# Optimization experiments

Hardware: AMD Instinct MI355X
Metric: run time of the kernel (lower is better)

## Reference

```python
import jax, jax.numpy as jnp
import numpy as np

DIM = 1024
NUM_HEADS = 16
NUM_KV_HEADS = 4
HEAD_DIM = DIM // NUM_HEADS
KV_DIM = NUM_KV_HEADS * HEAD_DIM
PARTIAL_ROPE_DIM = 32
ROPE_BASE = 10000.0
LORA_RANK = 4
NUM_LORA_STEPS = 2
LORA_SCALE = 1.0
B, S = 2, 2048


def _rms_norm(x):
    eps = jnp.asarray(jnp.finfo(x.dtype).eps, x.dtype)
    return x * jax.lax.rsqrt(jnp.mean(x * x, axis=-1, keepdims=True) + eps)


def _rope_cos_sin(seq_len, dtype):
    half = PARTIAL_ROPE_DIM // 2
    inv_freq = 1.0 / (ROPE_BASE ** (jnp.arange(0, PARTIAL_ROPE_DIM, 2, dtype=jnp.float32) / PARTIAL_ROPE_DIM))
    t = jnp.arange(seq_len, dtype=jnp.float32)
    freqs = jnp.outer(t, inv_freq)  # [S, half]
    return jnp.cos(freqs).astype(dtype), jnp.sin(freqs).astype(dtype)


def _apply_rope_partial(x, cos, sin):
    # x: [B, H, S, D]; rotate first PARTIAL_ROPE_DIM dims, pass the rest.
    half = PARTIAL_ROPE_DIM // 2
    x1 = x[..., :half]
    x2 = x[..., half:PARTIAL_ROPE_DIM]
    xp = x[..., PARTIAL_ROPE_DIM:]
    c = cos[None, None, :, :]
    s = sin[None, None, :, :]
    return jnp.concatenate([x1 * c + x2 * s, -x1 * s + x2 * c, xp], axis=-1)


def setup_inputs() -> dict:
    key = jax.random.key(0)
    ks = jax.random.split(key, 12)
    std = 0.02
    return {
        "x": jax.random.normal(ks[0], (B, S, DIM), jnp.float32),
        "Wq": jax.random.normal(ks[1], (DIM, DIM), jnp.float32) * std,
        "Wk": jax.random.normal(ks[2], (KV_DIM, DIM), jnp.float32) * std,
        "Wv": jax.random.normal(ks[3], (KV_DIM, DIM), jnp.float32) * std,
        "Wproj": jax.random.normal(ks[4], (DIM, DIM), jnp.float32) * std,
        "q_gain": jnp.full((NUM_HEADS,), 1.0, jnp.float32),
        "lora_A_q": jax.random.normal(ks[5], (NUM_LORA_STEPS, LORA_RANK, DIM), jnp.float32) * std,
        "lora_B_q": jax.random.normal(ks[6], (NUM_LORA_STEPS, DIM, LORA_RANK), jnp.float32) * std,
        "lora_A_v": jax.random.normal(ks[7], (NUM_LORA_STEPS, LORA_RANK, DIM), jnp.float32) * std,
        "lora_B_v": jax.random.normal(ks[8], (NUM_LORA_STEPS, KV_DIM, LORA_RANK), jnp.float32) * std,
        "step_idx": 0,
    }


def reference(x, Wq, Wk, Wv, Wproj, q_gain, lora_A_q, lora_B_q, lora_A_v, lora_B_v, step_idx):
    bsz, seqlen, dim = x.shape
    q = x @ Wq.T
    v = x @ Wv.T
    if 0 <= step_idx < NUM_LORA_STEPS:
        q = q + LORA_SCALE * ((x @ lora_A_q[step_idx].T) @ lora_B_q[step_idx].T)
        v = v + LORA_SCALE * ((x @ lora_A_v[step_idx].T) @ lora_B_v[step_idx].T)
    k = x @ Wk.T

    q = q.reshape(bsz, seqlen, NUM_HEADS, HEAD_DIM).transpose(0, 2, 1, 3)      # [B,H,S,D]
    k = k.reshape(bsz, seqlen, NUM_KV_HEADS, HEAD_DIM).transpose(0, 2, 1, 3)   # [B,Hkv,S,D]
    v = v.reshape(bsz, seqlen, NUM_KV_HEADS, HEAD_DIM).transpose(0, 2, 1, 3)

    q = _rms_norm(q)
    k = _rms_norm(k)

    cos, sin = _rope_cos_sin(seqlen, q.dtype)
    q = _apply_rope_partial(q, cos, sin)
    k = _apply_rope_partial(k, cos, sin)

    q = q * q_gain.astype(q.dtype)[None, :, None, None]

    # GQA causal SDPA
    groups = NUM_HEADS // NUM_KV_HEADS
    qg = q.reshape(bsz, NUM_KV_HEADS, groups, seqlen, HEAD_DIM)
    scale = 1.0 / np.sqrt(HEAD_DIM)
    scores = jnp.einsum('bkgsd,bktd->bkgst', qg, k) * scale  # [B,Hkv,G,S,S]
    causal = jnp.tril(jnp.ones((seqlen, seqlen), bool))
    scores = jnp.where(causal[None, None, None], scores, jnp.asarray(-jnp.inf, scores.dtype))
    attn = jax.nn.softmax(scores, axis=-1)
    y = jnp.einsum('bkgst,bktd->bkgsd', attn, v)
    y = y.reshape(bsz, NUM_HEADS, seqlen, HEAD_DIM).transpose(0, 2, 1, 3).reshape(bsz, seqlen, dim)
    return y @ Wproj.T
```

## Files before the change

kernel.cpp:

```cpp
#include <hip/hip_runtime.h>
#include <hip/hip_bf16.h>
#include <stdint.h>

#define DIM 1024
#define NH 16
#define NKV 4
#define HD 64
#define SEQ 2048
#define BATCH 2
#define RANK 4
#define NSTEPS 2

#define XN      4194304
#define WQ_END  5242880
#define WK_END  5505024
#define WV_END  5767168
#define CVT_BLOCKS 6656
#define LORA_BLOCKS 1024

typedef unsigned short u16;
typedef unsigned int u32;
typedef __attribute__((ext_vector_type(8))) __bf16 bf16x8;
typedef __attribute__((ext_vector_type(4))) float f32x4;

__device__ __forceinline__ float bf2f(u16 v) {
    u32 u = ((u32)v) << 16;
    return __builtin_bit_cast(float, u);
}
__device__ __forceinline__ u16 f2bf(float f) {
    u32 u = __builtin_bit_cast(u32, f);
    u32 r = (u + 0x7fffu + ((u >> 16) & 1u)) >> 16;
    return (u16)r;
}
__device__ __forceinline__ u32 pk2(float a, float b) {
    return (u32)f2bf(a) | ((u32)f2bf(b) << 16);
}
__device__ __forceinline__ u32 pk2t(float a, float b) {
    return __builtin_amdgcn_perm(__builtin_bit_cast(u32, b),
                                 __builtin_bit_cast(u32, a), 0x07060302u);
}
__device__ __forceinline__ void glds16(const u16* g, u16* l) {
    __builtin_amdgcn_global_load_lds(
        (const __attribute__((address_space(1))) u32*)g,
        (__attribute__((address_space(3))) u32*)l, 16, 0, 0);
}

__global__ __launch_bounds__(256) void k_prep(
    const float* __restrict__ x, const float* __restrict__ Wq,
    const float* __restrict__ Wk, const float* __restrict__ Wv,
    const float* __restrict__ Wp, u16* __restrict__ dst,
    const float* __restrict__ Aq, const float* __restrict__ Av,
    const int* __restrict__ step_p, float* __restrict__ tq, float* __restrict__ tv)
{
    int bx = blockIdx.x;
    if (bx < CVT_BLOCKS) {
        int e = (bx * 256 + threadIdx.x) * 4;
        const float* src;
        if (e < XN)          src = x  + e;
        else if (e < WQ_END) src = Wq + (e - XN);
        else if (e < WK_END) src = Wk + (e - WQ_END);
        else if (e < WV_END) src = Wv + (e - WK_END);
        else                 src = Wp + (e - WV_END);
        float4 v = *(const float4*)src;
        *(uint2*)(dst + e) = make_uint2(pk2(v.x, v.y), pk2(v.z, v.w));
        return;
    }
    int wave = ((bx - CVT_BLOCKS) * 256 + threadIdx.x) >> 6;
    int lane = threadIdx.x & 63;
    int step = step_p[0];
    int valid = (step >= 0 && step < NSTEPS);
    int sc = valid ? step : 0;
    const float* xr = x + wave * DIM + lane * 16;
    float xf[16];
#pragma unroll
    for (int q = 0; q < 4; q++) {
        float4 v4 = *(const float4*)(xr + q * 4);
        xf[q * 4 + 0] = v4.x; xf[q * 4 + 1] = v4.y;
        xf[q * 4 + 2] = v4.z; xf[q * 4 + 3] = v4.w;
    }
    float sums[8];
#pragma unroll
    for (int j = 0; j < 8; j++) {
        const float* ar = (j < 4 ? Aq + sc * RANK * DIM + j * DIM
                                 : Av + sc * RANK * DIM + (j - 4) * DIM) + lane * 16;
        float s = 0.f;
#pragma unroll
        for (int q = 0; q < 4; q++) {
            float4 a4 = *(const float4*)(ar + q * 4);
            s += xf[q * 4 + 0] * a4.x + xf[q * 4 + 1] * a4.y
               + xf[q * 4 + 2] * a4.z + xf[q * 4 + 3] * a4.w;
        }
#pragma unroll
        for (int o = 32; o > 0; o >>= 1) s += __shfl_xor(s, o, 64);
        sums[j] = s;
    }
    if (!valid) {
#pragma unroll
        for (int j = 0; j < 8; j++) sums[j] = 0.f;
    }
    if (lane == 0) {
        tq[wave * 4 + 0] = sums[0]; tq[wave * 4 + 1] = sums[1];
        tq[wave * 4 + 2] = sums[2]; tq[wave * 4 + 3] = sums[3];
        tv[wave * 4 + 0] = sums[4]; tv[wave * 4 + 1] = sums[5];
        tv[wave * 4 + 2] = sums[6]; tv[wave * 4 + 3] = sums[7];
    }
}

__global__ __launch_bounds__(256) void k_gemm_qkv(
    const u16* __restrict__ A, const u16* __restrict__ B,
    u16* __restrict__ qkv, u16* __restrict__ vtb,
    const float* __restrict__ tq, const float* __restrict__ Bq,
    const float* __restrict__ tv, const float* __restrict__ Bv,
    const float* __restrict__ gain, const int* __restrict__ step_p)
{
    __shared__ __align__(16) u16 As[8192];
    __shared__ __align__(16) u16 Bs[4096];
    __shared__ float sred[2][2][64];
    int bx = blockIdx.x;
    int bn = (bx & 7) * 3 + ((bx >> 3) % 3);
    int bm = (bx >> 3) / 3;
    int t = threadIdx.x, lane = t & 63, w = t >> 6;
    int wy = w >> 1, wx = w & 1;
    int wb = t & ~63;
    int quad = lane >> 4, n16 = lane & 15;
    f32x4 acc[4][2];
#pragma unroll
    for (int i = 0; i < 4; i++)
#pragma unroll
        for (int j = 0; j < 2; j++) acc[i][j] = (f32x4){0.f, 0.f, 0.f, 0.f};

    int goffA[4], goffB[2];
#pragma unroll
    for (int u = 0; u < 4; u++) {
        int idx = u * 256 + t;
        int grp = idx >> 6;
        int q_ = (idx >> 4) & 3, m = idx & 15;
        goffA[u] = ((grp >> 1) * 16 + m) * DIM + (grp & 1) * 32 + q_ * 8;
    }
#pragma unroll
    for (int u = 0; u < 2; u++) {
        int idx = u * 256 + t;
        int grp = idx >> 6;
        int q_ = (idx >> 4) & 3, m = idx & 15;
        goffB[u] = ((grp >> 1) * 16 + m) * DIM + (grp & 1) * 32 + q_ * 8;
    }
    const u16* Ab = A + bm * 128 * DIM;
    const u16* Bb = B + bn * 64 * DIM;

#pragma unroll 1
    for (int kb = 0; kb < 16; kb++) {
        int k0 = kb * 64;
        __syncthreads();
#pragma unroll
        for (int u = 0; u < 4; u++)
            glds16(Ab + goffA[u] + k0, As + (u * 256 + wb) * 8);
#pragma unroll
        for (int u = 0; u < 2; u++)
            glds16(Bb + goffB[u] + k0, Bs + (u * 256 + wb) * 8);
        __syncthreads();
#pragma unroll
        for (int c = 0; c < 2; c++) {
            bf16x8 af[4], bfr[2];
#pragma unroll
            for (int i = 0; i < 4; i++)
                af[i] = *(bf16x8*)(As + (((wy * 4 + i) * 2 + c) * 64 + lane) * 8);
#pragma unroll
            for (int j = 0; j < 2; j++)
                bfr[j] = *(bf16x8*)(Bs + (((wx * 2 + j) * 2 + c) * 64 + lane) * 8);
#pragma unroll
            for (int i = 0; i < 4; i++)
#pragma unroll
                for (int j = 0; j < 2; j++)
                    acc[i][j] = __builtin_amdgcn_mfma_f32_16x16x32_bf16(af[i], bfr[j], acc[i][j], 0, 0, 0);
        }
    }

    int step = step_p[0];
    int sc = (step >= 0 && step < NSTEPS) ? step : 0;
    int col_l0 = wx * 32 + n16;
    int row_base = bm * 128 + wy * 64 + quad * 4;

    if (bn < 20) {
        bool isq = (bn < 16);
        if (isq) {
            float4 B40 = *(const float4*)(Bq + (sc * DIM + bn * 64 + col_l0) * RANK);
            float4 B41 = *(const float4*)(Bq + (sc * DIM + bn * 64 + col_l0 + 16) * RANK);
#pragma unroll
            for (int i = 0; i < 4; i++)
#pragma unroll
                for (int r = 0; r < 4; r++) {
                    float4 t4 = *(const float4*)(tq + (row_base + i * 16 + r) * 4);
                    acc[i][0][r] += t4.x * B40.x + t4.y * B40.y + t4.z * B40.z + t4.w * B40.w;
                    acc[i][1][r] += t4.x * B41.x + t4.y * B41.y + t4.z * B41.z + t4.w * B41.w;
                }
        }
        float sq[4][4];
#pragma unroll
        for (int i = 0; i < 4; i++)
#pragma unroll
            for (int r = 0; r < 4; r++) {
                float s = acc[i][0][r] * acc[i][0][r] + acc[i][1][r] * acc[i][1][r];
#pragma unroll
                for (int o = 1; o < 16; o <<= 1) s += __shfl_xor(s, o, 64);
                sq[i][r] = s;
            }
        if (n16 == 0) {
#pragma unroll
            for (int i = 0; i < 4; i++)
#pragma unroll
                for (int r = 0; r < 4; r++)
                    sred[wy][wx][i * 16 + quad * 4 + r] = sq[i][r];
        }
        __syncthreads();
        float postmul = isq ? (gain[bn] * 0.125f * 1.4426950408889634f) : 1.f;
        int colbase = isq ? (bn * 64) : (1024 + (bn - 16) * 64);
        float invf = exp2f(-(float)n16 * 0.8304820237218405f);
#pragma unroll
        for (int i = 0; i < 4; i++)
#pragma unroll
            for (int r = 0; r < 4; r++) {
                int rl = i * 16 + quad * 4 + r;
                float total = sq[i][r] + sred[wy][wx ^ 1][rl];
                float rr = rsqrtf(total * (1.f / 64.f) + 1.1920928955078125e-7f);
                int row = bm * 128 + wy * 64 + rl;
                float v0 = acc[i][0][r] * rr, v1 = acc[i][1][r] * rr;
                float o0, o1;
                if (wx == 0) {
                    float ang = (float)(row & 2047) * invf;
                    float cs = cosf(ang), sn = sinf(ang);
                    o0 = v0 * cs + v1 * sn;
                    o1 = -v0 * sn + v1 * cs;
                } else {
                    o0 = v0; o1 = v1;
                }
                u16* dst = qkv + row * 1536 + colbase + col_l0;
                dst[0]  = f2bf(o0 * postmul);
                dst[16] = f2bf(o1 * postmul);
            }
    } else {
        int g = bn - 20;
        float4 B40 = *(const float4*)(Bv + (sc * (NKV * HD) + g * 64 + col_l0) * RANK);
        float4 B41 = *(const float4*)(Bv + (sc * (NKV * HD) + g * 64 + col_l0 + 16) * RANK);
#pragma unroll
        for (int i = 0; i < 4; i++) {
#pragma unroll
            for (int r = 0; r < 4; r++) {
                float4 t4 = *(const float4*)(tv + (row_base + i * 16 + r) * 4);
                acc[i][0][r] += t4.x * B40.x + t4.y * B40.y + t4.z * B40.z + t4.w * B40.w;
                acc[i][1][r] += t4.x * B41.x + t4.y * B41.y + t4.z * B41.z + t4.w * B41.w;
            }
            int row0 = row_base + i * 16;
            int b = row0 >> 11, s0 = row0 & 2047;
#pragma unroll
            for (int j = 0; j < 2; j++) {
                int d = col_l0 + j * 16;
                uint2 pkv = make_uint2(pk2(acc[i][j][0], acc[i][j][1]),
                                       pk2(acc[i][j][2], acc[i][j][3]));
                *(uint2*)(vtb + ((b * NKV + g) * HD + d) * SEQ + s0) = pkv;
            }
        }
    }
}

__global__ __launch_bounds__(256) void k_gemm_proj(
    const u16* __restrict__ A, const u16* __restrict__ B,
    float* __restrict__ C)
{
    __shared__ __align__(16) u16 As[8192];
    __shared__ __align__(16) u16 Bs[4096];
    int bx = blockIdx.x;
    int bn = (bx & 7) * 2 + ((bx >> 3) & 1);
    int bm = bx >> 4;
    int t = threadIdx.x, lane = t & 63, w = t >> 6;
    int wy = w >> 1, wx = w & 1;
    int wb = t & ~63;
    f32x4 acc[4][2];
#pragma unroll
    for (int i = 0; i < 4; i++)
#pragma unroll
        for (int j = 0; j < 2; j++) acc[i][j] = (f32x4){0.f, 0.f, 0.f, 0.f};

    int goffA[4], goffB[2];
#pragma unroll
    for (int u = 0; u < 4; u++) {
        int idx = u * 256 + t;
        int grp = idx >> 6;
        int q_ = (idx >> 4) & 3, m = idx & 15;
        goffA[u] = ((grp >> 1) * 16 + m) * DIM + (grp & 1) * 32 + q_ * 8;
    }
#pragma unroll
    for (int u = 0; u < 2; u++) {
        int idx = u * 256 + t;
        int grp = idx >> 6;
        int q_ = (idx >> 4) & 3, m = idx & 15;
        goffB[u] = ((grp >> 1) * 16 + m) * DIM + (grp & 1) * 32 + q_ * 8;
    }
    const u16* Ab = A + bm * 128 * DIM;
    const u16* Bb = B + bn * 64 * DIM;

#pragma unroll 1
    for (int kb = 0; kb < 16; kb++) {
        int k0 = kb * 64;
        __syncthreads();
#pragma unroll
        for (int u = 0; u < 4; u++)
            glds16(Ab + goffA[u] + k0, As + (u * 256 + wb) * 8);
#pragma unroll
        for (int u = 0; u < 2; u++)
            glds16(Bb + goffB[u] + k0, Bs + (u * 256 + wb) * 8);
        __syncthreads();
#pragma unroll
        for (int c = 0; c < 2; c++) {
            bf16x8 af[4], bfr[2];
#pragma unroll
            for (int i = 0; i < 4; i++)
                af[i] = *(bf16x8*)(As + (((wy * 4 + i) * 2 + c) * 64 + lane) * 8);
#pragma unroll
            for (int j = 0; j < 2; j++)
                bfr[j] = *(bf16x8*)(Bs + (((wx * 2 + j) * 2 + c) * 64 + lane) * 8);
#pragma unroll
            for (int i = 0; i < 4; i++)
#pragma unroll
                for (int j = 0; j < 2; j++)
                    acc[i][j] = __builtin_amdgcn_mfma_f32_16x16x32_bf16(af[i], bfr[j], acc[i][j], 0, 0, 0);
        }
    }
    int quad = lane >> 4, n16 = lane & 15;
#pragma unroll
    for (int i = 0; i < 4; i++)
#pragma unroll
        for (int j = 0; j < 2; j++) {
            int col = bn * 64 + wx * 32 + j * 16 + n16;
#pragma unroll
            for (int r = 0; r < 4; r++) {
                int rowm = bm * 128 + wy * 64 + i * 16 + quad * 4 + r;
                C[rowm * DIM + col] = acc[i][j][r];
            }
        }
}

__global__ __launch_bounds__(256) void k_attn(
    const u16* __restrict__ qkv, const u16* __restrict__ vt,
    const float* __restrict__ gain, u16* __restrict__ y,
    float* __restrict__ accP, float* __restrict__ psP)
{
    __shared__ __align__(16) u16 kf[4096];
    __shared__ __align__(16) u16 vf[4096];
    __shared__ __align__(16) u16 pb[4][1024];
    int bx = blockIdx.x;
    int bgid = bx & 7, inner = bx >> 3;
    int b = bgid >> 2, g = bgid & 3;
    int h = g * 4 + (inner & 3);
    int qtsel = (inner >> 2) & 15;
    int role = (inner >> 6) & 1;
    int pairsel = (b * 16 + h) * 16 + qtsel;
    int t = threadIdx.x, lane = t & 63, w = t >> 6, wb = t & ~63;
    int quad = lane >> 4, n16 = lane & 15;
    float negM = -11.67f * fabsf(gain[h]);

    const u16* kbase = qkv + b * SEQ * 1536 + 1024 + g * HD;
    const u16* vbase = vt + (b * NKV + g) * HD * SEQ;

    int koff0, koff1, voff0, voff1;
    {
        int s0 = t, r0 = s0 >> 3, c0 = (s0 & 7) ^ (r0 & 7);
        koff0 = r0 * 1536 + c0 * 8;  voff0 = r0 * 2048 + c0 * 8;
        int s1 = 256 + t, r1 = s1 >> 3, c1 = (s1 & 7) ^ (r1 & 7);
        koff1 = r1 * 1536 + c1 * 8;  voff1 = r1 * 2048 + c1 * 8;
    }
    int swb = n16 & 7;
    int o0 = n16 * 8 + (quad ^ swb);
    int o1 = n16 * 8 + ((4 + quad) ^ swb);
    u16* pw = pb[w];

    f32x4 acc[4];
    float ps;
    bf16x8 qlo, qhi;
    int qrow;

    auto reset_acc = [&]() {
#pragma unroll
        for (int i = 0; i < 4; i++) acc[i] = (f32x4){0.f, 0.f, 0.f, 0.f};
        ps = 0.f;
    };
    auto load_q = [&](int qt) {
        qrow = qt * 64 + w * 16 + n16;
        const u16* qp = qkv + (b * SEQ + qrow) * 1536 + h * HD + quad * 8;
        qlo = *(const bf16x8*)qp;
        qhi = *(const bf16x8*)(qp + 32);
    };
    auto tile = [&](int kt, bool diag) {
        __syncthreads();
        const u16* kp = kbase + kt * (64 * 1536);
        const u16* vp = vbase + kt * 64;
        glds16(kp + koff0, kf + wb * 8);
        glds16(kp + koff1, kf + (256 + wb) * 8);
        glds16(vp + voff0, vf + wb * 8);
        glds16(vp + voff1, vf + (256 + wb) * 8);
        __syncthreads();
        f32x4 st[4];
#pragma unroll
        for (int nt = 0; nt < 4; nt++) {
            f32x4 sa = (f32x4){0.f, 0.f, 0.f, 0.f};
            sa = __builtin_amdgcn_mfma_f32_16x16x32_bf16(*(bf16x8*)(kf + (nt * 128 + o0) * 8), qlo, sa, 0, 0, 0);
            sa = __builtin_amdgcn_mfma_f32_16x16x32_bf16(*(bf16x8*)(kf + (nt * 128 + o1) * 8), qhi, sa, 0, 0, 0);
            st[nt] = sa;
        }
        float p[4][4];
        if (diag) {
            int kb0 = kt * 64;
#pragma unroll
            for (int nt = 0; nt < 4; nt++)
#pragma unroll
                for (int r = 0; r < 4; r++) {
                    int key = kb0 + nt * 16 + quad * 4 + r;
                    float e = exp2f(st[nt][r] + negM);
                    e = (key > qrow) ? 0.f : e;
                    p[nt][r] = e;
                    ps += e;
                }
        } else {
#pragma unroll
            for (int nt = 0; nt < 4; nt++)
#pragma unroll
                for (int r = 0; r < 4; r++) {
                    float e = exp2f(st[nt][r] + negM);
                    p[nt][r] = e;
                    ps += e;
                }
        }
#pragma unroll
        for (int nt = 0; nt < 4; nt++) {
            u32 lo = pk2t(p[nt][0], p[nt][1]);
            u32 hi = pk2t(p[nt][2], p[nt][3]);
            int ck = nt >> 1;
            int qbk = (nt & 1) * 2 + (quad >> 1);
            int byteoff = (ck * 64 + qbk * 16 + n16) * 16 + (quad & 1) * 8;
            *(uint2*)((char*)pw + byteoff) = make_uint2(lo, hi);
        }
        asm volatile("s_waitcnt lgkmcnt(0)" ::: "memory");
#pragma unroll
        for (int ck = 0; ck < 2; ck++) {
            bf16x8 pfr = *(bf16x8*)(pw + (ck * 64 + lane) * 8);
            int oo = ck ? o1 : o0;
#pragma unroll
            for (int dt = 0; dt < 4; dt++)
                acc[dt] = __builtin_amdgcn_mfma_f32_16x16x32_bf16(*(bf16x8*)(vf + (dt * 128 + oo) * 8), pfr, acc[dt], 0, 0, 0);
        }
        asm volatile("" ::: "memory");
    };
    auto write_partial = [&](int pidx) {
        float pt = ps + __shfl_xor(ps, 16, 64);
        pt += __shfl_xor(pt, 32, 64);
        if (quad == 0) psP[pidx * 64 + w * 16 + n16] = pt;
        float* ap = accP + pidx * 4096 + w * 1024;
#pragma unroll
        for (int dt = 0; dt < 4; dt++)
#pragma unroll
            for (int r = 0; r < 4; r++)
                ap[dt * 256 + quad * 64 + r * 16 + n16] = acc[dt][r];
    };

    if (role == 0) {
        load_q(qtsel);
        reset_acc();
#pragma unroll 1
        for (int kt = 0; kt < qtsel; kt++) tile(kt, false);
        tile(qtsel, true);
        {
            float pt = ps + __shfl_xor(ps, 16, 64);
            pt += __shfl_xor(pt, 32, 64);
            float li = 1.f / pt;
#pragma unroll
            for (int dt = 0; dt < 4; dt++) {
                uint2 o = make_uint2(pk2(acc[dt][0] * li, acc[dt][1] * li),
                                     pk2(acc[dt][2] * li, acc[dt][3] * li));
                int d = dt * 16 + quad * 4;
                *(uint2*)(y + (b * SEQ + qrow) * DIM + h * HD + d) = o;
            }
        }
        load_q(31 - qtsel);
        reset_acc();
#pragma unroll 1
        for (int kt = 0; kt <= 15 - qtsel; kt++) tile(kt, false);
        write_partial(pairsel * 2);
    } else {
        load_q(31 - qtsel);
        reset_acc();
#pragma unroll 1
        for (int kt = 16 - qtsel; kt < 31 - qtsel; kt++) tile(kt, false);
        tile(31 - qtsel, true);
        write_partial(pairsel * 2 + 1);
    }
}

__global__ __launch_bounds__(256) void k_comb(
    const float* __restrict__ accP, const float* __restrict__ psP,
    u16* __restrict__ y)
{
    int pairsel = blockIdx.x;
    int b = pairsel >> 8, h = (pairsel >> 4) & 15, qtsel = pairsel & 15;
    int qt = 31 - qtsel;
    int t = threadIdx.x, w = t >> 6, d = t & 63;
    const float* a0 = accP + (pairsel * 2) * 4096 + t * 16;
    const float* a1 = a0 + 4096;
    const float* p0 = psP + pairsel * 128 + w * 16;
    const float* p1 = p0 + 64;
    u16* yp = y + (b * SEQ + qt * 64 + w * 16) * DIM + h * HD + d;
#pragma unroll
    for (int i = 0; i < 4; i++) {
        float4 v0 = *(const float4*)(a0 + i * 4);
        float4 v1 = *(const float4*)(a1 + i * 4);
        float4 s0 = *(const float4*)(p0 + i * 4);
        float4 s1 = *(const float4*)(p1 + i * 4);
        yp[(i * 4 + 0) * DIM] = f2bf((v0.x + v1.x) / (s0.x + s1.x));
        yp[(i * 4 + 1) * DIM] = f2bf((v0.y + v1.y) / (s0.y + s1.y));
        yp[(i * 4 + 2) * DIM] = f2bf((v0.z + v1.z) / (s0.z + s1.z));
        yp[(i * 4 + 3) * DIM] = f2bf((v0.w + v1.w) / (s0.w + s1.w));
    }
}

extern "C" void kernel_launch(void* const* d_in, const int* in_sizes, int n_in,
                              void* d_out, int out_size, void* d_ws, size_t ws_size,
                              hipStream_t stream)
{
    (void)in_sizes; (void)n_in; (void)out_size; (void)ws_size;
    const float* x     = (const float*)d_in[0];
    const float* Wq    = (const float*)d_in[1];
    const float* Wk    = (const float*)d_in[2];
    const float* Wv    = (const float*)d_in[3];
    const float* Wproj = (const float*)d_in[4];
    const float* qgain = (const float*)d_in[5];
    const float* Aq    = (const float*)d_in[6];
    const float* Bq    = (const float*)d_in[7];
    const float* Av    = (const float*)d_in[8];
    const float* Bv    = (const float*)d_in[9];
    const int*   step  = (const int*)d_in[10];

    char* ws = (char*)d_ws;
    u16* wsbf = (u16*)ws;
    u16* xb   = wsbf;
    u16* wf   = wsbf + XN;
    u16* wp   = wsbf + WV_END;
    u16* qkv  = (u16*)(ws + 13631488);
    float* tq = (float*)(ws + 26214400);
    float* tv = tq + 16384;
    float* psP = (float*)(ws + 26345472);
    u16* vt   = (u16*)(ws + 26607616);
    float* accP = (float*)d_out;
    u16* y    = xb;

    k_prep<<<CVT_BLOCKS + LORA_BLOCKS, 256, 0, stream>>>(x, Wq, Wk, Wv, Wproj, wsbf,
                                                         Aq, Av, step, tq, tv);
    k_gemm_qkv<<<768, 256, 0, stream>>>(xb, wf, qkv, vt, tq, Bq, tv, Bv, qgain, step);
    k_attn<<<1024, 256, 0, stream>>>(qkv, vt, qgain, y, accP, psP);
    k_comb<<<512, 256, 0, stream>>>(accP, psP, y);
    k_gemm_proj<<<512, 256, 0, stream>>>(y, wp, (float*)d_out);
}
```

Baseline: 216.4 us.

## Double-buffer LDS tiles in QKV and projection GEMMs to overlap loads with MFMA

Both GEMM kernels get double-buffered shared memory tiles. The next K-tile's global-to-LDS loads are issued before computing on the current tile, using a partial vmcnt wait and raw barriers. The goal is to hide global load latency behind MFMA work instead of stalling on two syncthreads per iteration. LDS use per block doubles, which may reduce occupancy, and correctness depends on the hand-counted vmcnt value.

```diff
diff --git a/kernel.cpp b/kernel.cpp
--- a/kernel.cpp
+++ b/kernel.cpp
@@ -113,8 +113,8 @@
     const float* __restrict__ tv, const float* __restrict__ Bv,
     const float* __restrict__ gain, const int* __restrict__ step_p)
 {
-    __shared__ __align__(16) u16 As[8192];
-    __shared__ __align__(16) u16 Bs[4096];
+    __shared__ __align__(16) u16 As[2][8192];
+    __shared__ __align__(16) u16 Bs[2][4096];
     __shared__ float sred[2][2][64];
     int bx = blockIdx.x;
     int bn = (bx & 7) * 3 + ((bx >> 3) % 3);
@@ -147,33 +147,47 @@
     const u16* Ab = A + bm * 128 * DIM;
     const u16* Bb = B + bn * 64 * DIM;
 
-#pragma unroll 1
-    for (int kb = 0; kb < 16; kb++) {
+    auto stage = [&](int kb, int pb_) {
         int k0 = kb * 64;
-        __syncthreads();
 #pragma unroll
         for (int u = 0; u < 4; u++)
-            glds16(Ab + goffA[u] + k0, As + (u * 256 + wb) * 8);
+            glds16(Ab + goffA[u] + k0, As[pb_] + (u * 256 + wb) * 8);
 #pragma unroll
         for (int u = 0; u < 2; u++)
-            glds16(Bb + goffB[u] + k0, Bs + (u * 256 + wb) * 8);
-        __syncthreads();
+            glds16(Bb + goffB[u] + k0, Bs[pb_] + (u * 256 + wb) * 8);
+    };
+    auto compute = [&](int pb_) {
+        const u16* Asc = As[pb_];
+        const u16* Bsc = Bs[pb_];
 #pragma unroll
         for (int c = 0; c < 2; c++) {
             bf16x8 af[4], bfr[2];
 #pragma unroll
             for (int i = 0; i < 4; i++)
-                af[i] = *(bf16x8*)(As + (((wy * 4 + i) * 2 + c) * 64 + lane) * 8);
+                af[i] = *(const bf16x8*)(Asc + (((wy * 4 + i) * 2 + c) * 64 + lane) * 8);
 #pragma unroll
             for (int j = 0; j < 2; j++)
-                bfr[j] = *(bf16x8*)(Bs + (((wx * 2 + j) * 2 + c) * 64 + lane) * 8);
+                bfr[j] = *(const bf16x8*)(Bsc + (((wx * 2 + j) * 2 + c) * 64 + lane) * 8);
 #pragma unroll
             for (int i = 0; i < 4; i++)
 #pragma unroll
                 for (int j = 0; j < 2; j++)
                     acc[i][j] = __builtin_amdgcn_mfma_f32_16x16x32_bf16(af[i], bfr[j], acc[i][j], 0, 0, 0);
         }
-    }
+    };
+
+    stage(0, 0);
+#pragma unroll 1
+    for (int kb = 0; kb < 15; kb++) {
+        stage(kb + 1, (kb + 1) & 1);
+        asm volatile("s_waitcnt vmcnt(6)" ::: "memory");
+        __builtin_amdgcn_s_barrier();
+        compute(kb & 1);
+        __builtin_amdgcn_s_barrier();
+    }
+    asm volatile("s_waitcnt vmcnt(0)" ::: "memory");
+    __builtin_amdgcn_s_barrier();
+    compute(1);
 
     int step = step_p[0];
     int sc = (step >= 0 && step < NSTEPS) ? step : 0;
@@ -266,8 +280,8 @@
     const u16* __restrict__ A, const u16* __restrict__ B,
     float* __restrict__ C)
 {
-    __shared__ __align__(16) u16 As[8192];
-    __shared__ __align__(16) u16 Bs[4096];
+    __shared__ __align__(16) u16 As[2][8192];
+    __shared__ __align__(16) u16 Bs[2][4096];
     int bx = blockIdx.x;
     int bn = (bx & 7) * 2 + ((bx >> 3) & 1);
     int bm = bx >> 4;
@@ -298,33 +312,48 @@
     const u16* Ab = A + bm * 128 * DIM;
     const u16* Bb = B + bn * 64 * DIM;
 
-#pragma unroll 1
-    for (int kb = 0; kb < 16; kb++) {
+    auto stage = [&](int kb, int pb_) {
         int k0 = kb * 64;
-        __syncthreads();
 #pragma unroll
         for (int u = 0; u < 4; u++)
-            glds16(Ab + goffA[u] + k0, As + (u * 256 + wb) * 8);
+            glds16(Ab + goffA[u] + k0, As[pb_] + (u * 256 + wb) * 8);
 #pragma unroll
         for (int u = 0; u < 2; u++)
-            glds16(Bb + goffB[u] + k0, Bs + (u * 256 + wb) * 8);
-        __syncthreads();
+            glds16(Bb + goffB[u] + k0, Bs[pb_] + (u * 256 + wb) * 8);
+    };
+    auto compute = [&](int pb_) {
+        const u16* Asc = As[pb_];
+        const u16* Bsc = Bs[pb_];
 #pragma unroll
         for (int c = 0; c < 2; c++) {
             bf16x8 af[4], bfr[2];
 #pragma unroll
             for (int i = 0; i < 4; i++)
-                af[i] = *(bf16x8*)(As + (((wy * 4 + i) * 2 + c) * 64 + lane) * 8);
+                af[i] = *(const bf16x8*)(Asc + (((wy * 4 + i) * 2 + c) * 64 + lane) * 8);
 #pragma unroll
             for (int j = 0; j < 2; j++)
-                bfr[j] = *(bf16x8*)(Bs + (((wx * 2 + j) * 2 + c) * 64 + lane) * 8);
+                bfr[j] = *(const bf16x8*)(Bsc + (((wx * 2 + j) * 2 + c) * 64 + lane) * 8);
 #pragma unroll
             for (int i = 0; i < 4; i++)
 #pragma unroll
                 for (int j = 0; j < 2; j++)
                     acc[i][j] = __builtin_amdgcn_mfma_f32_16x16x32_bf16(af[i], bfr[j], acc[i][j], 0, 0, 0);
         }
-    }
+    };
+
+    stage(0, 0);
+#pragma unroll 1
+    for (int kb = 0; kb < 15; kb++) {
+        stage(kb + 1, (kb + 1) & 1);
+        asm volatile("s_waitcnt vmcnt(6)" ::: "memory");
+        __builtin_amdgcn_s_barrier();
+        compute(kb & 1);
+        __builtin_amdgcn_s_barrier();
+    }
+    asm volatile("s_waitcnt vmcnt(0)" ::: "memory");
+    __builtin_amdgcn_s_barrier();
+    compute(1);
+
     int quad = lane >> 4, n16 = lane & 15;
 #pragma unroll
     for (int i = 0; i < 4; i++)
```

Result: slower. 228.6 us (+5.6%).

## Widen QKV GEMM tile to 128x128 so each wave owns a full head

Applied to the files above, without the earlier changes.

The fused QKV projection GEMM now uses 128x128 output tiles instead of 128x64, halving the grid to 384 blocks. Each wave covers 64 columns, a whole head, so the per-head RMS norm reduction runs inside a wave. This removes the cross-wave shared-memory exchange and the extra barrier, and B-tile loads are reused across more MFMAs. Block-to-tile mapping is also changed to group M tiles per XCD. The cost is more accumulator registers per thread (which may lower occupancy) and fewer blocks to spread across the CUs.

```diff
diff --git a/kernel.cpp b/kernel.cpp
--- a/kernel.cpp
+++ b/kernel.cpp
@@ -114,38 +114,31 @@
     const float* __restrict__ gain, const int* __restrict__ step_p)
 {
     __shared__ __align__(16) u16 As[8192];
-    __shared__ __align__(16) u16 Bs[4096];
-    __shared__ float sred[2][2][64];
+    __shared__ __align__(16) u16 Bs[8192];
     int bx = blockIdx.x;
-    int bn = (bx & 7) * 3 + ((bx >> 3) % 3);
-    int bm = (bx >> 3) / 3;
+    int xcd = bx & 7, o = bx >> 3;
+    int bm = xcd * 4 + (o & 3);
+    int bn = o >> 2;
     int t = threadIdx.x, lane = t & 63, w = t >> 6;
     int wy = w >> 1, wx = w & 1;
     int wb = t & ~63;
     int quad = lane >> 4, n16 = lane & 15;
-    f32x4 acc[4][2];
+    f32x4 acc[4][4];
 #pragma unroll
     for (int i = 0; i < 4; i++)
 #pragma unroll
-        for (int j = 0; j < 2; j++) acc[i][j] = (f32x4){0.f, 0.f, 0.f, 0.f};
-
-    int goffA[4], goffB[2];
+        for (int j = 0; j < 4; j++) acc[i][j] = (f32x4){0.f, 0.f, 0.f, 0.f};
+
+    int goff[4];
 #pragma unroll
     for (int u = 0; u < 4; u++) {
         int idx = u * 256 + t;
         int grp = idx >> 6;
         int q_ = (idx >> 4) & 3, m = idx & 15;
-        goffA[u] = ((grp >> 1) * 16 + m) * DIM + (grp & 1) * 32 + q_ * 8;
-    }
-#pragma unroll
-    for (int u = 0; u < 2; u++) {
-        int idx = u * 256 + t;
-        int grp = idx >> 6;
-        int q_ = (idx >> 4) & 3, m = idx & 15;
-        goffB[u] = ((grp >> 1) * 16 + m) * DIM + (grp & 1) * 32 + q_ * 8;
+        goff[u] = ((grp >> 1) * 16 + m) * DIM + (grp & 1) * 32 + q_ * 8;
     }
     const u16* Ab = A + bm * 128 * DIM;
-    const u16* Bb = B + bn * 64 * DIM;
+    const u16* Bb = B + bn * 128 * DIM;
 
 #pragma unroll 1
     for (int kb = 0; kb < 16; kb++) {
@@ -153,107 +146,97 @@
         __syncthreads();
 #pragma unroll
         for (int u = 0; u < 4; u++)
-            glds16(Ab + goffA[u] + k0, As + (u * 256 + wb) * 8);
-#pragma unroll
-        for (int u = 0; u < 2; u++)
-            glds16(Bb + goffB[u] + k0, Bs + (u * 256 + wb) * 8);
+            glds16(Ab + goff[u] + k0, As + (u * 256 + wb) * 8);
+#pragma unroll
+        for (int u = 0; u < 4; u++)
+            glds16(Bb + goff[u] + k0, Bs + (u * 256 + wb) * 8);
         __syncthreads();
 #pragma unroll
         for (int c = 0; c < 2; c++) {
-            bf16x8 af[4], bfr[2];
+            bf16x8 af[4], bfr[4];
 #pragma unroll
             for (int i = 0; i < 4; i++)
-                af[i] = *(bf16x8*)(As + (((wy * 4 + i) * 2 + c) * 64 + lane) * 8);
-#pragma unroll
-            for (int j = 0; j < 2; j++)
-                bfr[j] = *(bf16x8*)(Bs + (((wx * 2 + j) * 2 + c) * 64 + lane) * 8);
+                af[i] = *(const bf16x8*)(As + (((wy * 4 + i) * 2 + c) * 64 + lane) * 8);
+#pragma unroll
+            for (int j = 0; j < 4; j++)
+                bfr[j] = *(const bf16x8*)(Bs + (((wx * 4 + j) * 2 + c) * 64 + lane) * 8);
 #pragma unroll
             for (int i = 0; i < 4; i++)
 #pragma unroll
-                for (int j = 0; j < 2; j++)
+                for (int j = 0; j < 4; j++)
                     acc[i][j] = __builtin_amdgcn_mfma_f32_16x16x32_bf16(af[i], bfr[j], acc[i][j], 0, 0, 0);
         }
     }
 
     int step = step_p[0];
     int sc = (step >= 0 && step < NSTEPS) ? step : 0;
-    int col_l0 = wx * 32 + n16;
     int row_base = bm * 128 + wy * 64 + quad * 4;
 
-    if (bn < 20) {
-        bool isq = (bn < 16);
+    if (bn < 10) {
+        bool isq = (bn < 8);
+        int h2 = isq ? (bn * 2 + wx) : ((bn - 8) * 2 + wx);
+        int colbase = isq ? (h2 * 64) : (1024 + h2 * 64);
         if (isq) {
-            float4 B40 = *(const float4*)(Bq + (sc * DIM + bn * 64 + col_l0) * RANK);
-            float4 B41 = *(const float4*)(Bq + (sc * DIM + bn * 64 + col_l0 + 16) * RANK);
+            float4 B4[4];
+#pragma unroll
+            for (int j = 0; j < 4; j++)
+                B4[j] = *(const float4*)(Bq + (sc * DIM + h2 * 64 + j * 16 + n16) * RANK);
 #pragma unroll
             for (int i = 0; i < 4; i++)
 #pragma unroll
                 for (int r = 0; r < 4; r++) {
                     float4 t4 = *(const float4*)(tq + (row_base + i * 16 + r) * 4);
-                    acc[i][0][r] += t4.x * B40.x + t4.y * B40.y + t4.z * B40.z + t4.w * B40.w;
-                    acc[i][1][r] += t4.x * B41.x + t4.y * B41.y + t4.z * B41.z + t4.w * B41.w;
+#pragma unroll
+                    for (int j = 0; j < 4; j++)
+                        acc[i][j][r] += t4.x * B4[j].x + t4.y * B4[j].y
+                                      + t4.z * B4[j].z + t4.w * B4[j].w;
                 }
         }
-        float sq[4][4];
+        float postmul = isq ? (gain[h2] * 0.125f * 1.4426950408889634f) : 1.f;
+        float invf = exp2f(-(float)n16 * 0.8304820237218405f);
 #pragma unroll
         for (int i = 0; i < 4; i++)
 #pragma unroll
             for (int r = 0; r < 4; r++) {
-                float s = acc[i][0][r] * acc[i][0][r] + acc[i][1][r] * acc[i][1][r];
-#pragma unroll
-                for (int o = 1; o < 16; o <<= 1) s += __shfl_xor(s, o, 64);
-                sq[i][r] = s;
-            }
-        if (n16 == 0) {
-#pragma unroll
-            for (int i = 0; i < 4; i++)
-#pragma unroll
-                for (int r = 0; r < 4; r++)
-                    sred[wy][wx][i * 16 + quad * 4 + r] = sq[i][r];
-        }
-        __syncthreads();
-        float postmul = isq ? (gain[bn] * 0.125f * 1.4426950408889634f) : 1.f;
-        int colbase = isq ? (bn * 64) : (1024 + (bn - 16) * 64);
-        float invf = exp2f(-(float)n16 * 0.8304820237218405f);
-#pragma unroll
-        for (int i = 0; i < 4; i++)
-#pragma unroll
-            for (int r = 0; r < 4; r++) {
-                int rl = i * 16 + quad * 4 + r;
-                float total = sq[i][r] + sred[wy][wx ^ 1][rl];
-                float rr = rsqrtf(total * (1.f / 64.f) + 1.1920928955078125e-7f);
-                int row = bm * 128 + wy * 64 + rl;
+                float s = acc[i][0][r] * acc[i][0][r] + acc[i][1][r] * acc[i][1][r]
+                        + acc[i][2][r] * acc[i][2][r] + acc[i][3][r] * acc[i][3][r];
+#pragma unroll
+                for (int o2 = 1; o2 < 16; o2 <<= 1) s += __shfl_xor(s, o2, 64);
+                float rr = rsqrtf(s * (1.f / 64.f) + 1.1920928955078125e-7f);
+                int row = row_base + i * 16 + r;
                 float v0 = acc[i][0][r] * rr, v1 = acc[i][1][r] * rr;
-                float o0, o1;
-                if (wx == 0) {
-                    float ang = (float)(row & 2047) * invf;
-                    float cs = cosf(ang), sn = sinf(ang);
-                    o0 = v0 * cs + v1 * sn;
-                    o1 = -v0 * sn + v1 * cs;
-                } else {
-                    o0 = v0; o1 = v1;
-                }
-                u16* dst = qkv + row * 1536 + colbase + col_l0;
+                float v2 = acc[i][2][r] * rr, v3 = acc[i][3][r] * rr;
+                float ang = (float)(row & 2047) * invf;
+                float cs = cosf(ang), sn = sinf(ang);
+                float o0 = v0 * cs + v1 * sn;
+                float o1 = -v0 * sn + v1 * cs;
+                u16* dst = qkv + row * 1536 + colbase + n16;
                 dst[0]  = f2bf(o0 * postmul);
                 dst[16] = f2bf(o1 * postmul);
+                dst[32] = f2bf(v2 * postmul);
+                dst[48] = f2bf(v3 * postmul);
             }
     } else {
-        int g = bn - 20;
-        float4 B40 = *(const float4*)(Bv + (sc * (NKV * HD) + g * 64 + col_l0) * RANK);
-        float4 B41 = *(const float4*)(Bv + (sc * (NKV * HD) + g * 64 + col_l0 + 16) * RANK);
+        int g = (bn - 10) * 2 + wx;
+        float4 B4[4];
+#pragma unroll
+        for (int j = 0; j < 4; j++)
+            B4[j] = *(const float4*)(Bv + (sc * (NKV * HD) + g * 64 + j * 16 + n16) * RANK);
 #pragma unroll
         for (int i = 0; i < 4; i++) {
 #pragma unroll
             for (int r = 0; r < 4; r++) {
                 float4 t4 = *(const float4*)(tv + (row_base + i * 16 + r) * 4);
-                acc[i][0][r] += t4.x * B40.x + t4.y * B40.y + t4.z * B40.z + t4.w * B40.w;
-                acc[i][1][r] += t4.x * B41.x + t4.y * B41.y + t4.z * B41.z + t4.w * B41.w;
+#pragma unroll
+                for (int j = 0; j < 4; j++)
+                    acc[i][j][r] += t4.x * B4[j].x + t4.y * B4[j].y
+                                  + t4.z * B4[j].z + t4.w * B4[j].w;
             }
             int row0 = row_base + i * 16;
             int b = row0 >> 11, s0 = row0 & 2047;
 #pragma unroll
-            for (int j = 0; j < 2; j++) {
-                int d = col_l0 + j * 16;
+            for (int j = 0; j < 4; j++) {
+                int d = j * 16 + n16;
                 uint2 pkv = make_uint2(pk2(acc[i][j][0], acc[i][j][1]),
                                        pk2(acc[i][j][2], acc[i][j][3]));
                 *(uint2*)(vtb + ((b * NKV + g) * HD + d) * SEQ + s0) = pkv;
@@ -314,10 +297,10 @@
             bf16x8 af[4], bfr[2];
 #pragma unroll
             for (int i = 0; i < 4; i++)
-                af[i] = *(bf16x8*)(As + (((wy * 4 + i) * 2 + c) * 64 + lane) * 8);
+                af[i] = *(const bf16x8*)(As + (((wy * 4 + i) * 2 + c) * 64 + lane) * 8);
 #pragma unroll
             for (int j = 0; j < 2; j++)
-                bfr[j] = *(bf16x8*)(Bs + (((wx * 2 + j) * 2 + c) * 64 + lane) * 8);
+                bfr[j] = *(const bf16x8*)(Bs + (((wx * 2 + j) * 2 + c) * 64 + lane) * 8);
 #pragma unroll
             for (int i = 0; i < 4; i++)
 #pragma unroll
@@ -552,7 +535,7 @@
 
     k_prep<<<CVT_BLOCKS + LORA_BLOCKS, 256, 0, stream>>>(x, Wq, Wk, Wv, Wproj, wsbf,
                                                          Aq, Av, step, tq, tv);
-    k_gemm_qkv<<<768, 256, 0, stream>>>(xb, wf, qkv, vt, tq, Bq, tv, Bv, qgain, step);
+    k_gemm_qkv<<<384, 256, 0, stream>>>(xb, wf, qkv, vt, tq, Bq, tv, Bv, qgain, step);
     k_attn<<<1024, 256, 0, stream>>>(qkv, vt, qgain, y, accP, psP);
     k_comb<<<512, 256, 0, stream>>>(accP, psP, y);
     k_gemm_proj<<<512, 256, 0, stream>>>(y, wp, (float*)d_out);
```

After: 211.6 us. 2.3% less time.
